# Kernel optimization log

Hardware: AMD Instinct MI355X
Metric: run time of the kernel (lower is better)

## Reference

```python
import jax, jax.numpy as jnp
import numpy as np

N_NODES = 2048
N_ELEMS = 4096

# kind codes
KIND_R, KIND_IVS, KIND_VC, KIND_SW = 0, 1, 2, 3


def setup_inputs() -> dict:
    key = jax.random.key(0)
    k1, k2, k3 = jax.random.split(key, 3)
    M = jax.random.normal(k1, (N_NODES, N_ELEMS), dtype=jnp.float32)
    params = jax.random.uniform(k2, (N_ELEMS,), dtype=jnp.float32)
    kinds = jax.random.randint(k3, (N_ELEMS,), 0, 4, dtype=jnp.int32)
    return {"M": M, "params": params, "kinds": kinds}


def reference(M, params, kinds):
    N, E = M.shape
    W = 2 * E + N  # column width of every row block
    dt = M.dtype

    # kcl rows: [M | 0_{N,E} | 0_{N,N}]
    kcl = jnp.concatenate([M, jnp.zeros((N, E + N), dtype=dt)], axis=1)
    # kvl rows: [0_{E,E} | I_E | -M^T]
    kvl = jnp.concatenate(
        [jnp.zeros((E, E), dtype=dt), jnp.eye(E, dtype=dt), -M.T], axis=1
    )

    is_r = kinds == KIND_R
    is_ivs = kinds == KIND_IVS
    is_vc = kinds == KIND_VC
    is_sw = kinds == KIND_SW
    sw_on = params > 0

    one = jnp.ones((), dtype=dt)
    zero = jnp.zeros((), dtype=dt)
    # z-column value at pos: R -> -param, VC -> 1, SW(off) -> 1, else 0
    z_val = jnp.where(is_r, -params,
             jnp.where(is_vc | (is_sw & ~sw_on), one, zero)).astype(dt)
    # y-column value at E+pos: R -> 1, IVS -> 1, SW(on) -> 1, else 0
    y_val = jnp.where(is_r | is_ivs | (is_sw & sw_on), one, zero).astype(dt)

    pos = jnp.arange(E)
    elem = jnp.zeros((E, W), dtype=dt)
    elem = elem.at[pos, pos].set(z_val)
    elem = elem.at[pos, E + pos].set(y_val)

    return jnp.concatenate([kcl, kvl, elem], axis=0)
```

## Files before the change

### kernel.cpp

```cpp
#include <hip/hip_runtime.h>

#define NN 2048
#define EE 4096
#define WW 10240
#define TOT_ROWS 10240

typedef float v4f __attribute__((ext_vector_type(4)));

#define TP_BLOCKS 512

__device__ __forceinline__ void nt_store(float* p, v4f v) {
    __builtin_nontemporal_store(v, (v4f*)p);
}

__global__ __launch_bounds__(256) void coeff_kernel(
    const float* __restrict__ M,
    const float* __restrict__ params,
    const int*   __restrict__ kinds,
    float*       __restrict__ out)
{
    __shared__ __align__(16) float t[32 * 512];
    int tid = threadIdx.x;

    if (blockIdx.x < TP_BLOCKS) {
        int tpIdx = blockIdx.x;
        int cT = (tpIdx & 127) << 5;
        int rT = (tpIdx >> 7) << 9;

        #pragma unroll
        for (int pass = 0; pass < 16; ++pass) {
            int rr = pass * 32 + (tid >> 3);
            int c0 = (tid & 7) * 4;
            v4f val = *(const v4f*)(M + (size_t)(rT + rr) * EE + cT + c0);
            #pragma unroll
            for (int i = 0; i < 4; ++i) {
                int c = c0 + i;
                t[c * 512 + (rr ^ (c & 28))] = val[i];
            }
        }
        __syncthreads();

        #pragma unroll
        for (int pass = 0; pass < 16; ++pass) {
            int e   = pass * 2 + (tid >> 7);
            int rr0 = (tid & 127) * 4;
            v4f v = *(const v4f*)(&t[e * 512 + (rr0 ^ (e & 28))]);
            v4f nv = { -v[0], -v[1], -v[2], -v[3] };
            nt_store(out + (size_t)(NN + cT + e) * WW + 2 * EE + rT + rr0, nv);
        }
    } else {
        int row = blockIdx.x - TP_BLOCKS;
        int tid4 = tid * 4;
        float* dst = out + (size_t)row * WW;
        const v4f zero = {0.f, 0.f, 0.f, 0.f};

        if (row < NN) {
            const float* src = M + (size_t)row * EE;
            #pragma unroll
            for (int k = 0; k < 4; ++k) {
                int off = k * 1024 + tid4;
                nt_store(dst + off, *(const v4f*)(src + off));
            }
            #pragma unroll
            for (int k = 4; k < 10; ++k)
                nt_store(dst + k * 1024 + tid4, zero);
        } else if (row < NN + EE) {
            int e = row - NN;
            int col_y = EE + e;
            #pragma unroll
            for (int k = 0; k < 8; ++k) {
                int base = k * 1024 + tid4;
                v4f v = zero;
                #pragma unroll
                for (int j = 0; j < 4; ++j)
                    if (base + j == col_y) v[j] = 1.0f;
                nt_store(dst + base, v);
            }
        } else {
            int e = row - (NN + EE);
            float p = params[e];
            int kk = kinds[e];
            bool on = p > 0.0f;
            float z, y;
            if (kk == 0)      { z = -p;             y = 1.0f; }
            else if (kk == 1) { z = 0.0f;           y = 1.0f; }
            else if (kk == 2) { z = 1.0f;           y = 0.0f; }
            else              { z = on ? 0.f : 1.f; y = on ? 1.f : 0.f; }
            int col_z = e, col_y = EE + e;
            #pragma unroll
            for (int k = 0; k < 10; ++k) {
                int base = k * 1024 + tid4;
                v4f v = zero;
                #pragma unroll
                for (int j = 0; j < 4; ++j) {
                    if (base + j == col_z) v[j] = z;
                    if (base + j == col_y) v[j] = y;
                }
                nt_store(dst + base, v);
            }
        }
    }
}

extern "C" void kernel_launch(void* const* d_in, const int* in_sizes, int n_in,
                              void* d_out, int out_size, void* d_ws, size_t ws_size,
                              hipStream_t stream) {
    const float* M      = (const float*)d_in[0];
    const float* params = (const float*)d_in[1];
    const int*   kinds  = (const int*)d_in[2];
    float*       out    = (float*)d_out;

    coeff_kernel<<<TP_BLOCKS + TOT_ROWS, 256, 0, stream>>>(M, params, kinds, out);
}
```

Baseline: 425.1 us.

## Merge transpose and row-fill work into 512 persistent blocks

Instead of launching 512 transpose blocks plus one block per output row, each of 512 blocks now does one transpose tile and then writes 20 full rows (4 kcl, 8 kvl, 8 elem) strided by 512. This cuts block launch and scheduling overhead and evens out the work per block. In exchange there are far fewer blocks (512 at 256 threads, with 64KB of shared memory each), which limits occupancy and memory-level parallelism for a store-bound kernel. Each block's row writes also wait until its transpose phase finishes.

```diff
diff --git a/kernel.cpp b/kernel.cpp
--- a/kernel.cpp
+++ b/kernel.cpp
@@ -7,7 +7,7 @@
 
 typedef float v4f __attribute__((ext_vector_type(4)));
 
-#define TP_BLOCKS 512
+#define NBLK 512
 
 __device__ __forceinline__ void nt_store(float* p, v4f v) {
     __builtin_nontemporal_store(v, (v4f*)p);
@@ -21,11 +21,11 @@
 {
     __shared__ __align__(16) float t[32 * 512];
     int tid = threadIdx.x;
+    int b = blockIdx.x;
 
-    if (blockIdx.x < TP_BLOCKS) {
-        int tpIdx = blockIdx.x;
-        int cT = (tpIdx & 127) << 5;
-        int rT = (tpIdx >> 7) << 9;
+    {
+        int cT = (b & 127) << 5;
+        int rT = (b >> 7) << 9;
 
         #pragma unroll
         for (int pass = 0; pass < 16; ++pass) {
@@ -48,56 +48,67 @@
             v4f nv = { -v[0], -v[1], -v[2], -v[3] };
             nt_store(out + (size_t)(NN + cT + e) * WW + 2 * EE + rT + rr0, nv);
         }
-    } else {
-        int row = blockIdx.x - TP_BLOCKS;
-        int tid4 = tid * 4;
+    }
+
+    int tid4 = tid * 4;
+    const v4f zero = {0.f, 0.f, 0.f, 0.f};
+
+    #pragma unroll
+    for (int k2 = 0; k2 < 4; ++k2) {
+        int row = b + NBLK * k2;
         float* dst = out + (size_t)row * WW;
-        const v4f zero = {0.f, 0.f, 0.f, 0.f};
+        const float* src = M + (size_t)row * EE;
+        #pragma unroll
+        for (int k = 0; k < 4; ++k) {
+            int off = k * 1024 + tid4;
+            nt_store(dst + off, *(const v4f*)(src + off));
+        }
+        #pragma unroll
+        for (int k = 4; k < 10; ++k)
+            nt_store(dst + k * 1024 + tid4, zero);
+    }
 
-        if (row < NN) {
-            const float* src = M + (size_t)row * EE;
+    #pragma unroll
+    for (int k2 = 4; k2 < 12; ++k2) {
+        int row = b + NBLK * k2;
+        int e = row - NN;
+        int col_y = EE + e;
+        float* dst = out + (size_t)row * WW;
+        #pragma unroll
+        for (int k = 0; k < 8; ++k) {
+            int base = k * 1024 + tid4;
+            v4f v = zero;
             #pragma unroll
-            for (int k = 0; k < 4; ++k) {
-                int off = k * 1024 + tid4;
-                nt_store(dst + off, *(const v4f*)(src + off));
+            for (int j = 0; j < 4; ++j)
+                if (base + j == col_y) v[j] = 1.0f;
+            nt_store(dst + base, v);
+        }
+    }
+
+    #pragma unroll
+    for (int k2 = 12; k2 < 20; ++k2) {
+        int row = b + NBLK * k2;
+        int e = row - (NN + EE);
+        float p = params[e];
+        int kk = kinds[e];
+        bool on = p > 0.0f;
+        float z, y;
+        if (kk == 0)      { z = -p;             y = 1.0f; }
+        else if (kk == 1) { z = 0.0f;           y = 1.0f; }
+        else if (kk == 2) { z = 1.0f;           y = 0.0f; }
+        else              { z = on ? 0.f : 1.f; y = on ? 1.f : 0.f; }
+        int col_z = e, col_y = EE + e;
+        float* dst = out + (size_t)row * WW;
+        #pragma unroll
+        for (int k = 0; k < 10; ++k) {
+            int base = k * 1024 + tid4;
+            v4f v = zero;
+            #pragma unroll
+            for (int j = 0; j < 4; ++j) {
+                if (base + j == col_z) v[j] = z;
+                if (base + j == col_y) v[j] = y;
             }
-            #pragma unroll
-            for (int k = 4; k < 10; ++k)
-                nt_store(dst + k * 1024 + tid4, zero);
-        } else if (row < NN + EE) {
-            int e = row - NN;
-            int col_y = EE + e;
-            #pragma unroll
-            for (int k = 0; k < 8; ++k) {
-                int base = k * 1024 + tid4;
-                v4f v = zero;
-                #pragma unroll
-                for (int j = 0; j < 4; ++j)
-                    if (base + j == col_y) v[j] = 1.0f;
-                nt_store(dst + base, v);
-            }
-        } else {
-            int e = row - (NN + EE);
-            float p = params[e];
-            int kk = kinds[e];
-            bool on = p > 0.0f;
-            float z, y;
-            if (kk == 0)      { z = -p;             y = 1.0f; }
-            else if (kk == 1) { z = 0.0f;           y = 1.0f; }
-            else if (kk == 2) { z = 1.0f;           y = 0.0f; }
-            else              { z = on ? 0.f : 1.f; y = on ? 1.f : 0.f; }
-            int col_z = e, col_y = EE + e;
-            #pragma unroll
-            for (int k = 0; k < 10; ++k) {
-                int base = k * 1024 + tid4;
-                v4f v = zero;
-                #pragma unroll
-                for (int j = 0; j < 4; ++j) {
-                    if (base + j == col_z) v[j] = z;
-                    if (base + j == col_y) v[j] = y;
-                }
-                nt_store(dst + base, v);
-            }
+            nt_store(dst + base, v);
         }
     }
 }
@@ -110,5 +121,5 @@
     const int*   kinds  = (const int*)d_in[2];
     float*       out    = (float*)d_out;
 
-    coeff_kernel<<<TP_BLOCKS + TOT_ROWS, 256, 0, stream>>>(M, params, kinds, out);
+    coeff_kernel<<<NBLK, 256, 0, stream>>>(M, params, kinds, out);
 }
```

Measured after the change: 430.4 us. Within noise of the previous version (+1.2%).
